# Kernel optimization log

Hardware: AMD Instinct MI355X
Metric: run time of the kernel (lower is better)

Reference implementation:

```python
import jax, jax.numpy as jnp
import numpy as np

B, N, H, HID, LOCALITY = 2, 4096, 4, 256, 30.0
VD = HID // H
F32_MAX = jnp.finfo(jnp.float32).max


def setup_inputs() -> dict:
    key = jax.random.key(0)
    k1, k2, k3, k4 = jax.random.split(key, 4)
    m_dist = jax.random.uniform(k1, (B, N, N), dtype=jnp.float32)  # pairwise distances (b,N,N)
    x = jax.random.normal(k2, (B, N, HID), dtype=jnp.float32)
    r = jax.random.normal(k3, (1, H, 1, 1), dtype=jnp.float32)  # learned per-head distance scale
    # lecun_normal: std = 1/sqrt(fan_in), fan_in = HID
    weight = jax.random.normal(k4, (H, HID, VD), dtype=jnp.float32) / np.sqrt(HID)
    return {"m_dist": m_dist, "x": x, "r": r, "weight": weight}


def reference(m_dist, x, r, weight):
    # scaled distance per head: (b,h,n,n)
    scaled = m_dist[:, None, :, :] * (r ** 2)
    # percentile-thresholded local mask (linear interpolation, per row)
    thresh = jnp.percentile(scaled, LOCALITY, axis=-1, keepdims=True, method="linear")
    scaled = jnp.where(scaled <= thresh, scaled, F32_MAX)
    att = jax.nn.softmax(-scaled, axis=-1)  # (b,h,n,n)
    value = jnp.einsum("bnj,hjk->bhnk", x, weight)  # (b,h,n,v)
    out = jnp.einsum("bhnj,bhjd->bhnd", att, value)  # (b,h,n,v)
    out = jnp.transpose(out, (0, 2, 1, 3)).reshape(out.shape[0], -1, HID)  # (b,n,hid)
    return jax.nn.gelu(out, approximate=False)
```

## Files before the change

### kernel.cpp

```cpp
#include <hip/hip_runtime.h>
#include <hip/hip_bf16.h>

#define Bc   2
#define Nc   4096
#define Hc   4
#define HIDc 256
#define VDc  64

typedef short s8v  __attribute__((ext_vector_type(8)));
typedef float f4v  __attribute__((ext_vector_type(4)));

#define XSP 260

__global__ __launch_bounds__(256) void value_kernel(
    const float* __restrict__ x, const float* __restrict__ wgt,
    unsigned short* __restrict__ vt_g)
{
    __shared__ float xs[64 * XSP];
    __shared__ unsigned short ob[64 * 64];

    int t  = threadIdx.x;
    int bid = blockIdx.x;
    int nt = bid & 63;
    int h  = (bid >> 6) & 3;
    int b  = bid >> 8;
    int n0 = nt * 64;

    const float* xg = x + ((size_t)b * Nc + n0) * HIDc;
    #pragma unroll
    for (int i = 0; i < 16; i++) {
        int id = t + i * 256;
        int row = id >> 6, ch = id & 63;
        *(float4*)&xs[row * XSP + ch * 4] = ((const float4*)xg)[id];
    }
    __syncthreads();

    int k4 = t & 15;
    int ns = t >> 4;
    const float4* wg4 = (const float4*)(wgt + (size_t)h * HIDc * VDc);

    float4 acc[4];
    #pragma unroll
    for (int i = 0; i < 4; i++) acc[i] = (float4){0.f, 0.f, 0.f, 0.f};

    for (int j = 0; j < HIDc; j += 4) {
        float4 w0 = wg4[(j + 0) * 16 + k4];
        float4 w1 = wg4[(j + 1) * 16 + k4];
        float4 w2 = wg4[(j + 2) * 16 + k4];
        float4 w3 = wg4[(j + 3) * 16 + k4];
        #pragma unroll
        for (int i = 0; i < 4; i++) {
            float4 xv = *(const float4*)&xs[(ns + i * 16) * XSP + j];
            acc[i].x += xv.x * w0.x + xv.y * w1.x + xv.z * w2.x + xv.w * w3.x;
            acc[i].y += xv.x * w0.y + xv.y * w1.y + xv.z * w2.y + xv.w * w3.y;
            acc[i].z += xv.x * w0.z + xv.y * w1.z + xv.z * w2.z + xv.w * w3.z;
            acc[i].w += xv.x * w0.w + xv.y * w1.w + xv.z * w2.w + xv.w * w3.w;
        }
    }
    #pragma unroll
    for (int i = 0; i < 4; i++) {
        int nn = ns + i * 16;
        float a[4] = {acc[i].x, acc[i].y, acc[i].z, acc[i].w};
        #pragma unroll
        for (int c = 0; c < 4; c++) {
            __hip_bfloat16 hb = __float2bfloat16(a[c]);
            ob[(k4 * 4 + c) * 64 + nn] = *(unsigned short*)&hb;
        }
    }
    __syncthreads();

    unsigned short* vg = vt_g + (((size_t)b * Hc + h) * VDc) * Nc + n0;
    #pragma unroll
    for (int i = 0; i < 16; i++) {
        int idx = t + i * 256;
        int kk = idx >> 6, nn = idx & 63;
        vg[(size_t)kk * Nc + nn] = ob[idx];
    }
}

__global__ __launch_bounds__(256) void thresh_kernel(
    const float* __restrict__ m_dist,
    float* __restrict__ thr_out, float* __restrict__ min_out)
{
    __shared__ unsigned int hist[1024];
    __shared__ float wred[4];
    __shared__ unsigned int wscan[4];
    __shared__ int b0s, b1s;
    __shared__ unsigned int c0s;
    __shared__ unsigned int ncand;
    __shared__ float cand[256];
    __shared__ float s0s, s1s;

    int t = threadIdx.x;
    size_t rowid = blockIdx.x;
    const float* row = m_dist + rowid * Nc;

    for (int i = t; i < 1024; i += 256) hist[i] = 0u;
    if (t == 0) ncand = 0u;
    __syncthreads();

    float4 vals[4];
    float lmin = 1e30f;
    #pragma unroll
    for (int i = 0; i < 4; i++) {
        float4 v = ((const float4*)row)[t + i * 256];
        vals[i] = v;
        lmin = fminf(lmin, fminf(fminf(v.x, v.y), fminf(v.z, v.w)));
        atomicAdd(&hist[min(1023, (int)(v.x * 1024.0f))], 1u);
        atomicAdd(&hist[min(1023, (int)(v.y * 1024.0f))], 1u);
        atomicAdd(&hist[min(1023, (int)(v.z * 1024.0f))], 1u);
        atomicAdd(&hist[min(1023, (int)(v.w * 1024.0f))], 1u);
    }
    #pragma unroll
    for (int o = 32; o > 0; o >>= 1) lmin = fminf(lmin, __shfl_xor(lmin, o));
    if ((t & 63) == 0) wred[t >> 6] = lmin;
    __syncthreads();
    float rmin = fminf(fminf(wred[0], wred[1]), fminf(wred[2], wred[3]));

    unsigned int c[4], csum = 0;
    #pragma unroll
    for (int j = 0; j < 4; j++) { c[j] = hist[t * 4 + j]; csum += c[j]; }
    unsigned int inc = csum;
    #pragma unroll
    for (int o = 1; o < 64; o <<= 1) {
        unsigned int nv = __shfl_up(inc, o);
        if ((t & 63) >= o) inc += nv;
    }
    if ((t & 63) == 63) wscan[t >> 6] = inc;
    __syncthreads();
    unsigned int wpref = 0;
    for (int wv = 0; wv < (t >> 6); wv++) wpref += wscan[wv];
    unsigned int P = wpref + inc - csum;

    const unsigned int R0 = 1228u, R1 = 1229u;
    unsigned int cum = P;
    #pragma unroll
    for (int j = 0; j < 4; j++) {
        unsigned int lo = cum, hi = cum + c[j];
        if (R0 >= lo && R0 < hi) { b0s = t * 4 + j; c0s = lo; }
        if (R1 >= lo && R1 < hi) { b1s = t * 4 + j; }
        cum = hi;
    }
    __syncthreads();
    int b0 = b0s, b1 = b1s;
    unsigned int C0 = c0s;

    #pragma unroll
    for (int i = 0; i < 4; i++) {
        float a[4] = {vals[i].x, vals[i].y, vals[i].z, vals[i].w};
        #pragma unroll
        for (int j = 0; j < 4; j++) {
            int bx = min(1023, (int)(a[j] * 1024.0f));
            if (bx >= b0 && bx <= b1) {
                unsigned int p = atomicAdd(&ncand, 1u);
                if (p < 256u) cand[p] = a[j];
            }
        }
    }
    __syncthreads();
    unsigned int nc = min(ncand, 256u);
    if ((unsigned int)t < nc) {
        float v = cand[t];
        unsigned int rk = C0;
        for (unsigned int j = 0; j < nc; j++) {
            float u = cand[j];
            rk += (u < v || (u == v && j < (unsigned int)t)) ? 1u : 0u;
        }
        if (rk == R0) s0s = v;
        if (rk == R1) s1s = v;
    }
    __syncthreads();
    if (t == 0) {
        thr_out[rowid] = 0.5f * (s0s + s1s);
        min_out[rowid] = rmin;
    }
}

#define NT 32
#define JT 64
#define BIGF 3.0e38f

__global__ __launch_bounds__(512, 8) void attn_kernel(
    const float* __restrict__ m_dist, const float* __restrict__ rr,
    const unsigned short* __restrict__ vt_g,
    const float* __restrict__ thr_g, const float* __restrict__ min_g,
    float* __restrict__ Op, float* __restrict__ Zp, int jlen)
{
    __shared__ float ms[NT * 64];
    __shared__ unsigned short vt[Hc * VDc * 64];

    int t = threadIdx.x;
    const int nblk = Bc * (Nc / NT);
    int js = blockIdx.x / nblk;
    int rb = blockIdx.x - js * nblk;
    int b  = rb >> 7;
    int n0 = (rb & 127) * NT;
    int j0 = js * jlen;

    int lane = t & 63, q = lane >> 4, m16 = lane & 15;
    int w = t >> 6;
    int h = w & 3, rh = w >> 2;
    int row = rh * 16 + m16;

    float mn = min_g[b * Nc + n0 + row];
    float rv = rr[h];
    float cc = -(rv * rv) * 1.4426950408889634f;
    float nmncc = -mn * cc;

    f4v acc[4];
    #pragma unroll
    for (int ct = 0; ct < 4; ct++) acc[ct] = (f4v){0.f, 0.f, 0.f, 0.f};
    float zacc = 0.f;

    const float* mbase = m_dist + ((size_t)b * Nc + n0) * Nc + j0;
    const unsigned short* vtb = vt_g + ((size_t)b * Hc * VDc) * Nc + j0;

    int mrow = t >> 4, mch = t & 15;
    int msw  = mrow * 64 + ((mch ^ (mrow & 15)) << 2);
    float thm = thr_g[b * Nc + n0 + mrow];
    int vrow0 = t >> 3, vch = t & 7;

    int a00 = row * 64 + (((q * 2 + 0) ^ m16) << 2);
    int a01 = row * 64 + (((q * 2 + 1) ^ m16) << 2);
    int a10 = row * 64 + (((8 + q * 2 + 0) ^ m16) << 2);
    int a11 = row * 64 + (((8 + q * 2 + 1) ^ m16) << 2);

    for (int jt = 0; jt < jlen; jt += JT) {
        {
            float4 v = *(const float4*)(mbase + (size_t)mrow * Nc + jt + mch * 4);
            v.x = (v.x <= thm) ? v.x : BIGF;
            v.y = (v.y <= thm) ? v.y : BIGF;
            v.z = (v.z <= thm) ? v.z : BIGF;
            v.w = (v.w <= thm) ? v.w : BIGF;
            *(float4*)&ms[msw] = v;
        }
        #pragma unroll
        for (int i = 0; i < 4; i++) {
            int rrow = vrow0 + i * 64;
            *(float4*)&vt[rrow * 64 + ((vch ^ (rrow & 7)) << 3)] =
                *(const float4*)(vtb + (size_t)rrow * Nc + jt + vch * 8);
        }
        __syncthreads();

        const unsigned short* vb = &vt[(h * VDc) * 64];
        #pragma unroll
        for (int ks = 0; ks < 2; ks++) {
            float4 a0 = *(const float4*)&ms[ks ? a10 : a00];
            float4 a1 = *(const float4*)&ms[ks ? a11 : a01];
            float w0 = __builtin_amdgcn_exp2f(__builtin_fmaf(a0.x, cc, nmncc));
            float w1 = __builtin_amdgcn_exp2f(__builtin_fmaf(a0.y, cc, nmncc));
            float w2 = __builtin_amdgcn_exp2f(__builtin_fmaf(a0.z, cc, nmncc));
            float w3 = __builtin_amdgcn_exp2f(__builtin_fmaf(a0.w, cc, nmncc));
            float w4 = __builtin_amdgcn_exp2f(__builtin_fmaf(a1.x, cc, nmncc));
            float w5 = __builtin_amdgcn_exp2f(__builtin_fmaf(a1.y, cc, nmncc));
            float w6 = __builtin_amdgcn_exp2f(__builtin_fmaf(a1.z, cc, nmncc));
            float w7 = __builtin_amdgcn_exp2f(__builtin_fmaf(a1.w, cc, nmncc));
            zacc += ((w0 + w1) + (w2 + w3)) + ((w4 + w5) + (w6 + w7));
            union { s8v v; __hip_bfloat162 h2[4]; } afu;
            afu.h2[0] = __float22bfloat162_rn((float2){w0, w1});
            afu.h2[1] = __float22bfloat162_rn((float2){w2, w3});
            afu.h2[2] = __float22bfloat162_rn((float2){w4, w5});
            afu.h2[3] = __float22bfloat162_rn((float2){w6, w7});
            #pragma unroll
            for (int ct = 0; ct < 4; ct++) {
                int brow = ct * 16 + m16;
                s8v bf = *(const s8v*)(vb + brow * 64 + (((ks * 4 + q) ^ (m16 & 7)) << 3));
                acc[ct] = __builtin_amdgcn_mfma_f32_16x16x32_bf16(afu.v, bf, acc[ct], 0, 0, 0);
            }
        }
        __syncthreads();
    }

    zacc += __shfl_xor(zacc, 16);
    zacc += __shfl_xor(zacc, 32);
    if (q == 0)
        Zp[(((size_t)js * Bc + b) * Hc + h) * Nc + n0 + row] = zacc;

    #pragma unroll
    for (int ct = 0; ct < 4; ct++) {
        #pragma unroll
        for (int rg = 0; rg < 4; rg++) {
            int nl = rh * 16 + q * 4 + rg;
            Op[(((size_t)js * Bc + b) * Nc + n0 + nl) * HIDc + h * VDc + ct * 16 + m16]
                = acc[ct][rg];
        }
    }
}

__global__ __launch_bounds__(256) void combine_kernel(
    const float* __restrict__ Op, const float* __restrict__ Zp,
    float* __restrict__ out, int S)
{
    int g = blockIdx.x * 256 + threadIdx.x;
    int c4 = g & 63;
    int n  = (g >> 6) & (Nc - 1);
    int b  = g >> 18;
    int h  = c4 >> 4;

    float z = 0.f;
    float4 v = {0.f, 0.f, 0.f, 0.f};
    for (int s = 0; s < S; s++) {
        z += Zp[(((size_t)s * Bc + b) * Hc + h) * Nc + n];
        float4 p = *(const float4*)&Op[(((size_t)s * Bc + b) * Nc + n) * HIDc + c4 * 4];
        v.x += p.x; v.y += p.y; v.z += p.z; v.w += p.w;
    }
    float iz = 1.0f / z;
    float4 o;
    float u;
    u = v.x * iz; o.x = 0.5f * u * (1.0f + erff(u * 0.7071067811865476f));
    u = v.y * iz; o.y = 0.5f * u * (1.0f + erff(u * 0.7071067811865476f));
    u = v.z * iz; o.z = 0.5f * u * (1.0f + erff(u * 0.7071067811865476f));
    u = v.w * iz; o.w = 0.5f * u * (1.0f + erff(u * 0.7071067811865476f));
    *(float4*)&out[(((size_t)b * Nc + n) * HIDc) + c4 * 4] = o;
}

extern "C" void kernel_launch(void* const* d_in, const int* in_sizes, int n_in,
                              void* d_out, int out_size, void* d_ws, size_t ws_size,
                              hipStream_t stream) {
    const float* m_dist = (const float*)d_in[0];
    const float* x      = (const float*)d_in[1];
    const float* r      = (const float*)d_in[2];
    const float* weight = (const float*)d_in[3];
    float* out = (float*)d_out;

    char* ws = (char*)d_ws;
    const size_t MB = 1024 * 1024;
    unsigned short* vt = (unsigned short*)ws;
    float* thr = (float*)(ws + 4 * MB);
    float* mn  = (float*)(ws + 4 * MB + 32 * 1024);
    float* Zp  = (float*)(ws + 4 * MB + 64 * 1024);
    float* Op  = (float*)(ws + 5 * MB);

    int S = 4;
    if (ws_size < 5 * MB + 4 * (size_t)(Bc * Nc * HIDc * 4)) S = 2;
    if (ws_size < 5 * MB + 2 * (size_t)(Bc * Nc * HIDc * 4)) S = 1;
    int jlen = Nc / S;

    value_kernel<<<512, 256, 0, stream>>>(x, weight, vt);
    thresh_kernel<<<Bc * Nc, 256, 0, stream>>>(m_dist, thr, mn);
    attn_kernel<<<S * Bc * (Nc / NT), 512, 0, stream>>>(m_dist, r, vt, thr, mn, Op, Zp, jlen);
    combine_kernel<<<(Bc * Nc * HIDc) / 1024, 256, 0, stream>>>(Op, Zp, out, S);
}
```

Baseline: 277.4 us.

## Split attention K-dim across waves, reuse V fragments, privatize threshold histograms

The attention kernel now assigns each wave both 16-row halves of the 32-row tile but only half of the 64-wide j chunk. The four V fragments are loaded from LDS once per tile and reused for both row halves. The two j-halves' partial accumulators and normalizers are reduced through shared memory, and the output tile is staged so global stores become coalesced float4 writes. This doubles accumulator registers, lowers the occupancy hint from 8 to 6, and adds an extra reduction step with barriers. Separately, the threshold kernel gives each wave its own histogram to reduce LDS atomic contention.

```diff
diff --git a/kernel.cpp b/kernel.cpp
--- a/kernel.cpp
+++ b/kernel.cpp
@@ -82,7 +82,7 @@
     const float* __restrict__ m_dist,
     float* __restrict__ thr_out, float* __restrict__ min_out)
 {
-    __shared__ unsigned int hist[1024];
+    __shared__ unsigned int hist[4][1024];
     __shared__ float wred[4];
     __shared__ unsigned int wscan[4];
     __shared__ int b0s, b1s;
@@ -92,10 +92,11 @@
     __shared__ float s0s, s1s;
 
     int t = threadIdx.x;
+    int wid = t >> 6;
     size_t rowid = blockIdx.x;
     const float* row = m_dist + rowid * Nc;
 
-    for (int i = t; i < 1024; i += 256) hist[i] = 0u;
+    for (int i = t; i < 4096; i += 256) ((unsigned int*)hist)[i] = 0u;
     if (t == 0) ncand = 0u;
     __syncthreads();
 
@@ -106,30 +107,34 @@
         float4 v = ((const float4*)row)[t + i * 256];
         vals[i] = v;
         lmin = fminf(lmin, fminf(fminf(v.x, v.y), fminf(v.z, v.w)));
-        atomicAdd(&hist[min(1023, (int)(v.x * 1024.0f))], 1u);
-        atomicAdd(&hist[min(1023, (int)(v.y * 1024.0f))], 1u);
-        atomicAdd(&hist[min(1023, (int)(v.z * 1024.0f))], 1u);
-        atomicAdd(&hist[min(1023, (int)(v.w * 1024.0f))], 1u);
+        atomicAdd(&hist[wid][min(1023, (int)(v.x * 1024.0f))], 1u);
+        atomicAdd(&hist[wid][min(1023, (int)(v.y * 1024.0f))], 1u);
+        atomicAdd(&hist[wid][min(1023, (int)(v.z * 1024.0f))], 1u);
+        atomicAdd(&hist[wid][min(1023, (int)(v.w * 1024.0f))], 1u);
     }
     #pragma unroll
     for (int o = 32; o > 0; o >>= 1) lmin = fminf(lmin, __shfl_xor(lmin, o));
-    if ((t & 63) == 0) wred[t >> 6] = lmin;
+    if ((t & 63) == 0) wred[wid] = lmin;
     __syncthreads();
     float rmin = fminf(fminf(wred[0], wred[1]), fminf(wred[2], wred[3]));
 
     unsigned int c[4], csum = 0;
     #pragma unroll
-    for (int j = 0; j < 4; j++) { c[j] = hist[t * 4 + j]; csum += c[j]; }
+    for (int j = 0; j < 4; j++) {
+        int bin = t * 4 + j;
+        c[j] = hist[0][bin] + hist[1][bin] + hist[2][bin] + hist[3][bin];
+        csum += c[j];
+    }
     unsigned int inc = csum;
     #pragma unroll
     for (int o = 1; o < 64; o <<= 1) {
         unsigned int nv = __shfl_up(inc, o);
         if ((t & 63) >= o) inc += nv;
     }
-    if ((t & 63) == 63) wscan[t >> 6] = inc;
+    if ((t & 63) == 63) wscan[wid] = inc;
     __syncthreads();
     unsigned int wpref = 0;
-    for (int wv = 0; wv < (t >> 6); wv++) wpref += wscan[wv];
+    for (int wv = 0; wv < wid; wv++) wpref += wscan[wv];
     unsigned int P = wpref + inc - csum;
 
     const unsigned int R0 = 1228u, R1 = 1229u;
@@ -179,15 +184,19 @@
 #define NT 32
 #define JT 64
 #define BIGF 3.0e38f
-
-__global__ __launch_bounds__(512, 8) void attn_kernel(
+#define OBP 260
+
+__global__ __launch_bounds__(512, 6) void attn_kernel(
     const float* __restrict__ m_dist, const float* __restrict__ rr,
     const unsigned short* __restrict__ vt_g,
     const float* __restrict__ thr_g, const float* __restrict__ min_g,
     float* __restrict__ Op, float* __restrict__ Zp, int jlen)
 {
-    __shared__ float ms[NT * 64];
-    __shared__ unsigned short vt[Hc * VDc * 64];
+    __shared__ __align__(16) unsigned char lds[40960];
+    float* ms = (float*)lds;
+    unsigned short* vt = (unsigned short*)(lds + 8192);
+    float* obuf = (float*)lds;
+    float* zs = (float*)(lds + 33280);
 
     int t = threadIdx.x;
     const int nblk = Bc * (Nc / NT);
@@ -199,18 +208,18 @@
 
     int lane = t & 63, q = lane >> 4, m16 = lane & 15;
     int w = t >> 6;
-    int h = w & 3, rh = w >> 2;
-    int row = rh * 16 + m16;
-
-    float mn = min_g[b * Nc + n0 + row];
+    int h = w & 3, jh = w >> 2;
+
+    float mn0 = min_g[b * Nc + n0 + m16];
+    float mn1 = min_g[b * Nc + n0 + 16 + m16];
     float rv = rr[h];
     float cc = -(rv * rv) * 1.4426950408889634f;
-    float nmncc = -mn * cc;
-
-    f4v acc[4];
-    #pragma unroll
-    for (int ct = 0; ct < 4; ct++) acc[ct] = (f4v){0.f, 0.f, 0.f, 0.f};
-    float zacc = 0.f;
+    float nm0 = -mn0 * cc, nm1 = -mn1 * cc;
+
+    f4v acc[8];
+    #pragma unroll
+    for (int i = 0; i < 8; i++) acc[i] = (f4v){0.f, 0.f, 0.f, 0.f};
+    float zacc0 = 0.f, zacc1 = 0.f;
 
     const float* mbase = m_dist + ((size_t)b * Nc + n0) * Nc + j0;
     const unsigned short* vtb = vt_g + ((size_t)b * Hc * VDc) * Nc + j0;
@@ -220,10 +229,11 @@
     float thm = thr_g[b * Nc + n0 + mrow];
     int vrow0 = t >> 3, vch = t & 7;
 
-    int a00 = row * 64 + (((q * 2 + 0) ^ m16) << 2);
-    int a01 = row * 64 + (((q * 2 + 1) ^ m16) << 2);
-    int a10 = row * 64 + (((8 + q * 2 + 0) ^ m16) << 2);
-    int a11 = row * 64 + (((8 + q * 2 + 1) ^ m16) << 2);
+    int ac0 = ((jh * 8 + q * 2 + 0) ^ m16) << 2;
+    int ac1 = ((jh * 8 + q * 2 + 1) ^ m16) << 2;
+    int row0 = m16 * 64, row1 = (16 + m16) * 64;
+    int boff = (((jh * 4 + q) ^ (m16 & 7)) << 3);
+    const unsigned short* vb = &vt[h * VDc * 64];
 
     for (int jt = 0; jt < jlen; jt += JT) {
         {
@@ -242,48 +252,80 @@
         }
         __syncthreads();
 
-        const unsigned short* vb = &vt[(h * VDc) * 64];
-        #pragma unroll
-        for (int ks = 0; ks < 2; ks++) {
-            float4 a0 = *(const float4*)&ms[ks ? a10 : a00];
-            float4 a1 = *(const float4*)&ms[ks ? a11 : a01];
-            float w0 = __builtin_amdgcn_exp2f(__builtin_fmaf(a0.x, cc, nmncc));
-            float w1 = __builtin_amdgcn_exp2f(__builtin_fmaf(a0.y, cc, nmncc));
-            float w2 = __builtin_amdgcn_exp2f(__builtin_fmaf(a0.z, cc, nmncc));
-            float w3 = __builtin_amdgcn_exp2f(__builtin_fmaf(a0.w, cc, nmncc));
-            float w4 = __builtin_amdgcn_exp2f(__builtin_fmaf(a1.x, cc, nmncc));
-            float w5 = __builtin_amdgcn_exp2f(__builtin_fmaf(a1.y, cc, nmncc));
-            float w6 = __builtin_amdgcn_exp2f(__builtin_fmaf(a1.z, cc, nmncc));
-            float w7 = __builtin_amdgcn_exp2f(__builtin_fmaf(a1.w, cc, nmncc));
-            zacc += ((w0 + w1) + (w2 + w3)) + ((w4 + w5) + (w6 + w7));
+        s8v bf0 = *(const s8v*)(vb + (0 * 16 + m16) * 64 + boff);
+        s8v bf1 = *(const s8v*)(vb + (1 * 16 + m16) * 64 + boff);
+        s8v bf2 = *(const s8v*)(vb + (2 * 16 + m16) * 64 + boff);
+        s8v bf3 = *(const s8v*)(vb + (3 * 16 + m16) * 64 + boff);
+
+        #pragma unroll
+        for (int rh = 0; rh < 2; rh++) {
+            float4 a0 = *(const float4*)&ms[(rh ? row1 : row0) + ac0];
+            float4 a1 = *(const float4*)&ms[(rh ? row1 : row0) + ac1];
+            float nm = rh ? nm1 : nm0;
+            float w0 = __builtin_amdgcn_exp2f(__builtin_fmaf(a0.x, cc, nm));
+            float w1 = __builtin_amdgcn_exp2f(__builtin_fmaf(a0.y, cc, nm));
+            float w2 = __builtin_amdgcn_exp2f(__builtin_fmaf(a0.z, cc, nm));
+            float w3 = __builtin_amdgcn_exp2f(__builtin_fmaf(a0.w, cc, nm));
+            float w4 = __builtin_amdgcn_exp2f(__builtin_fmaf(a1.x, cc, nm));
+            float w5 = __builtin_amdgcn_exp2f(__builtin_fmaf(a1.y, cc, nm));
+            float w6 = __builtin_amdgcn_exp2f(__builtin_fmaf(a1.z, cc, nm));
+            float w7 = __builtin_amdgcn_exp2f(__builtin_fmaf(a1.w, cc, nm));
+            float zz = ((w0 + w1) + (w2 + w3)) + ((w4 + w5) + (w6 + w7));
+            if (rh) zacc1 += zz; else zacc0 += zz;
             union { s8v v; __hip_bfloat162 h2[4]; } afu;
             afu.h2[0] = __float22bfloat162_rn((float2){w0, w1});
             afu.h2[1] = __float22bfloat162_rn((float2){w2, w3});
             afu.h2[2] = __float22bfloat162_rn((float2){w4, w5});
             afu.h2[3] = __float22bfloat162_rn((float2){w6, w7});
+            acc[rh * 4 + 0] = __builtin_amdgcn_mfma_f32_16x16x32_bf16(afu.v, bf0, acc[rh * 4 + 0], 0, 0, 0);
+            acc[rh * 4 + 1] = __builtin_amdgcn_mfma_f32_16x16x32_bf16(afu.v, bf1, acc[rh * 4 + 1], 0, 0, 0);
+            acc[rh * 4 + 2] = __builtin_amdgcn_mfma_f32_16x16x32_bf16(afu.v, bf2, acc[rh * 4 + 2], 0, 0, 0);
+            acc[rh * 4 + 3] = __builtin_amdgcn_mfma_f32_16x16x32_bf16(afu.v, bf3, acc[rh * 4 + 3], 0, 0, 0);
+        }
+        __syncthreads();
+    }
+
+    zacc0 += __shfl_xor(zacc0, 16); zacc0 += __shfl_xor(zacc0, 32);
+    zacc1 += __shfl_xor(zacc1, 16); zacc1 += __shfl_xor(zacc1, 32);
+    if (lane < 16) {
+        zs[((h * 2 + jh) * 2 + 0) * 16 + m16] = zacc0;
+        zs[((h * 2 + jh) * 2 + 1) * 16 + m16] = zacc1;
+    }
+    if (jh == 0) {
+        #pragma unroll
+        for (int rh = 0; rh < 2; rh++)
             #pragma unroll
-            for (int ct = 0; ct < 4; ct++) {
-                int brow = ct * 16 + m16;
-                s8v bf = *(const s8v*)(vb + brow * 64 + (((ks * 4 + q) ^ (m16 & 7)) << 3));
-                acc[ct] = __builtin_amdgcn_mfma_f32_16x16x32_bf16(afu.v, bf, acc[ct], 0, 0, 0);
-            }
-        }
-        __syncthreads();
-    }
-
-    zacc += __shfl_xor(zacc, 16);
-    zacc += __shfl_xor(zacc, 32);
-    if (q == 0)
-        Zp[(((size_t)js * Bc + b) * Hc + h) * Nc + n0 + row] = zacc;
-
-    #pragma unroll
-    for (int ct = 0; ct < 4; ct++) {
-        #pragma unroll
-        for (int rg = 0; rg < 4; rg++) {
-            int nl = rh * 16 + q * 4 + rg;
-            Op[(((size_t)js * Bc + b) * Nc + n0 + nl) * HIDc + h * VDc + ct * 16 + m16]
-                = acc[ct][rg];
-        }
+            for (int ct = 0; ct < 4; ct++)
+                #pragma unroll
+                for (int rg = 0; rg < 4; rg++)
+                    obuf[(rh * 16 + q * 4 + rg) * OBP + h * VDc + ct * 16 + m16]
+                        = acc[rh * 4 + ct][rg];
+    }
+    __syncthreads();
+    if (jh == 1) {
+        #pragma unroll
+        for (int rh = 0; rh < 2; rh++)
+            #pragma unroll
+            for (int ct = 0; ct < 4; ct++)
+                #pragma unroll
+                for (int rg = 0; rg < 4; rg++) {
+                    int o = (rh * 16 + q * 4 + rg) * OBP + h * VDc + ct * 16 + m16;
+                    obuf[o] += acc[rh * 4 + ct][rg];
+                }
+    } else if (lane < 16) {
+        float za = zs[((h * 2 + 0) * 2 + 0) * 16 + m16] + zs[((h * 2 + 1) * 2 + 0) * 16 + m16];
+        float zb = zs[((h * 2 + 0) * 2 + 1) * 16 + m16] + zs[((h * 2 + 1) * 2 + 1) * 16 + m16];
+        size_t zb0 = (((size_t)js * Bc + b) * Hc + h) * Nc + n0;
+        Zp[zb0 + m16] = za;
+        Zp[zb0 + 16 + m16] = zb;
+    }
+    __syncthreads();
+    float* opg = &Op[(((size_t)js * Bc + b) * Nc + n0) * HIDc];
+    #pragma unroll
+    for (int i = 0; i < 4; i++) {
+        int fid = i * 512 + t;
+        int r_ = fid >> 6, c_ = (fid & 63) * 4;
+        *(float4*)&opg[r_ * HIDc + c_] = *(float4*)&obuf[r_ * OBP + c_];
     }
 }
 
```

Result: slower. 327.6 us (+18.1%).
